# Kernel optimization log

Measured on AMD Instinct MI355X. Metric: run time of the kernel, lower is better.

The kernel has to match this reference:

```python
import jax, jax.numpy as jnp
import numpy as np

DIM = 768
NUM_HEADS = 12
HEAD_DIM = DIM // NUM_HEADS  # 64


def setup_inputs() -> dict:
    key = jax.random.key(0)
    k1, k2, k3, k4 = jax.random.split(key, 4)
    B, N = 2, 2048
    x = jax.random.normal(k1, (B, N, DIM), dtype=jnp.float32)
    att_mask = jnp.ones((B, N), dtype=jnp.int32)
    # learned params (qkv has no bias since qkv_bias=False)
    qkv_w = jax.random.normal(k2, (3 * DIM, DIM), dtype=jnp.float32) * (1.0 / np.sqrt(DIM))
    proj_w = jax.random.normal(k3, (DIM, DIM), dtype=jnp.float32) * (1.0 / np.sqrt(DIM))
    proj_b = jax.random.normal(k4, (DIM,), dtype=jnp.float32) * 0.02
    return {"x": x, "att_mask": att_mask, "qkv_w": qkv_w, "proj_w": proj_w, "proj_b": proj_b}


def reference(x, att_mask, qkv_w, proj_w, proj_b):
    B, N, C = x.shape
    H, Dh = NUM_HEADS, HEAD_DIM
    scale = Dh ** (-0.5)
    # qkv projection: [B,N,3C] -> [3,B,H,N,Dh]
    qkv = jnp.einsum('bnc,oc->bno', x, qkv_w)
    qkv = qkv.reshape(B, N, 3, H, Dh).transpose(2, 0, 3, 1, 4)
    q, k, v = qkv[0], qkv[1], qkv[2]
    q = q * scale
    # full N x N logits (the memory-bound hotspot)
    logit = jnp.einsum('bhnd,bhmd->bhnm', q, k)
    # 2D mask path: [B,N] -> [B,1,1,N], masked_fill(mask==0, -inf)
    mask = att_mask[:, None, None, :]
    logit = jnp.where(mask == 0, -jnp.inf, logit)
    attn = jax.nn.softmax(logit, axis=-1)  # attn_drop is identity (p=0, eval)
    out = jnp.einsum('bhnm,bhmd->bhnd', attn, v)
    out = out.transpose(0, 2, 1, 3).reshape(B, N, H * Dh)
    out = jnp.einsum('bnc,oc->bno', out, proj_w) + proj_b  # proj_drop identity
    return out
```

## Files before the change

kernel.cpp:

```cpp
#include <hip/hip_runtime.h>
#include <hip/hip_bf16.h>
#include <math.h>
#include <cstdint>
#include <cstddef>

typedef __bf16 bf16x8 __attribute__((ext_vector_type(8)));
typedef __bf16 bf16x4 __attribute__((ext_vector_type(4)));
typedef short  s16x4  __attribute__((ext_vector_type(4)));
typedef float  f32x4  __attribute__((ext_vector_type(4)));

#define GLOAD16(g, l) __builtin_amdgcn_global_load_lds( \
    (const __attribute__((address_space(1))) void*)(g),  \
    (__attribute__((address_space(3))) void*)(l), 16, 0, 0)

__device__ __forceinline__ unsigned short f2bf(float f) {
    union { float f; unsigned u; } v; v.f = f;
    unsigned u = v.u;
    u += 0x7fffu + ((u >> 16) & 1u);
    return (unsigned short)(u >> 16);
}

__device__ __forceinline__ unsigned pack_bf16x2(float a, float b) {
    __hip_bfloat162 h = __float22bfloat162_rn(make_float2(a, b));
    return *reinterpret_cast<unsigned*>(&h);
}

__device__ __forceinline__ f32x4 mfma16(bf16x4 a, bf16x4 b, f32x4 c) {
#if __has_builtin(__builtin_amdgcn_mfma_f32_16x16x16_bf16)
    return __builtin_amdgcn_mfma_f32_16x16x16_bf16(a, b, c, 0, 0, 0);
#elif __has_builtin(__builtin_amdgcn_mfma_f32_16x16x16bf16_1k)
    return __builtin_amdgcn_mfma_f32_16x16x16bf16_1k(
        __builtin_bit_cast(s16x4, a), __builtin_bit_cast(s16x4, b), c, 0, 0, 0);
#else
    asm volatile("v_mfma_f32_16x16x16_bf16 %0, %1, %2, %0"
                 : "+v"(c) : "v"(a), "v"(b));
    return c;
#endif
}

__global__ __launch_bounds__(256) void cvt_all(
    const float* __restrict__ x,
    const float* __restrict__ qkvw,
    const float* __restrict__ projw,
    unsigned short* __restrict__ xb,
    unsigned short* __restrict__ wqkv,
    unsigned short* __restrict__ wproj)
{
    const int N1 = 4096 * 768;
    const int N2 = 2304 * 768;
    const int SC = 768 * 768;
    const float C2 = 0.18033688011112042f;
    int i = ((int)blockIdx.x * 256 + (int)threadIdx.x) * 4;

    const float* src;
    unsigned short* dst;
    int j;
    bool sc = false;
    if (i < N1)           { src = x;     dst = xb;    j = i; }
    else if (i < N1 + N2) { j = i - N1;  src = qkvw;  dst = wqkv;  sc = (j < SC); }
    else                  { j = i - N1 - N2; src = projw; dst = wproj; }

    float4 v = *reinterpret_cast<const float4*>(src + j);
    if (sc) { v.x *= C2; v.y *= C2; v.z *= C2; v.w *= C2; }
    uint2 pk;
    pk.x = pack_bf16x2(v.x, v.y);
    pk.y = pack_bf16x2(v.z, v.w);
    *reinterpret_cast<uint2*>(dst + j) = pk;
}

template <int MODE, int MROWS, int NF>
__global__ __launch_bounds__(256) void gemm_bt(
    const unsigned short* __restrict__ A,
    const unsigned short* __restrict__ B,
    unsigned short* __restrict__ Cb,
    unsigned short* __restrict__ Vt,
    float* __restrict__ Cf,
    const float* __restrict__ bias,
    int M, int N, int K)
{
    constexpr int MI = MROWS / 32;
    __shared__ __align__(16) unsigned short Al[2][MROWS * 64];
    __shared__ __align__(16) unsigned short Bl[2][NF * 32 * 64];
    const int bm   = blockIdx.x * MROWS;
    const int bn   = blockIdx.y * (NF * 32);
    const int tid  = (int)threadIdx.x;
    const int wave = tid >> 6;
    const int lane = tid & 63;
    const int wr   = wave >> 1;
    const int wc   = wave & 1;
    const int q    = lane & 15;
    const int g4   = (lane >> 4) * 4;

    f32x4 acc[MI][NF] = {};

    const int srow = lane >> 3;
    const int scol = (lane & 7) * 8;

    auto stage = [&](int buf, int k0) {
#pragma unroll
        for (int i = 0; i < MI; ++i) {
            const int chunk = wave * MI + i;
            GLOAD16(A + (size_t)(bm + chunk * 8 + srow) * K + (k0 + scol),
                    &Al[buf][chunk * 512]);
        }
#pragma unroll
        for (int i = 0; i < NF; ++i) {
            const int chunk = wave * NF + i;
            GLOAD16(B + (size_t)(bn + chunk * 8 + srow) * K + (k0 + scol),
                    &Bl[buf][chunk * 512]);
        }
    };

    stage(0, 0);
    __syncthreads();

    const int nt = K / 64;
    int buf = 0;
    for (int t = 0; t < nt; ++t) {
        if (t + 1 < nt) stage(buf ^ 1, (t + 1) * 64);
#pragma unroll
        for (int kk = 0; kk < 2; ++kk) {
            const int ko = kk * 32 + (lane >> 4) * 8;
            bf16x8 af[MI], bf[NF];
#pragma unroll
            for (int mi = 0; mi < MI; ++mi)
                af[mi] = *(const bf16x8*)&Al[buf][(wr * (MROWS / 2) + mi * 16 + q) * 64 + ko];
#pragma unroll
            for (int ni = 0; ni < NF; ++ni)
                bf[ni] = *(const bf16x8*)&Bl[buf][(wc * 16 * NF + ni * 16 + q) * 64 + ko];
#pragma unroll
            for (int mi = 0; mi < MI; ++mi)
#pragma unroll
                for (int ni = 0; ni < NF; ++ni)
                    acc[mi][ni] = __builtin_amdgcn_mfma_f32_16x16x32_bf16(
                        af[mi], bf[ni], acc[mi][ni], 0, 0, 0);
        }
        __syncthreads();
        buf ^= 1;
    }

#pragma unroll
    for (int mi = 0; mi < MI; ++mi) {
        const int row0 = bm + wr * (MROWS / 2) + mi * 16 + g4;
        if constexpr (MODE == 1) {
#pragma unroll
            for (int ni = 0; ni < NF; ++ni) {
                const int col = bn + wc * 16 * NF + ni * 16 + q;
#pragma unroll
                for (int r = 0; r < 4; ++r)
                    Cf[(size_t)(row0 + r) * N + col] = acc[mi][ni][r] + bias[col];
            }
        } else {
            if (bn < 1536) {
#pragma unroll
                for (int ni = 0; ni < NF; ++ni) {
                    const int col = bn + wc * 16 * NF + ni * 16 + q;
#pragma unroll
                    for (int r = 0; r < 4; ++r)
                        Cb[(size_t)(row0 + r) * 1536 + col] = f2bf(acc[mi][ni][r]);
                }
            } else {
                const int b  = row0 >> 11;
                const int np = row0 & 2047;
#pragma unroll
                for (int ni = 0; ni < NF; ++ni) {
                    const int vcol = bn + wc * 16 * NF + ni * 16 + q - 1536;
                    const int hv = vcol >> 6, d = vcol & 63;
                    uint2 w;
                    w.x = pack_bf16x2(acc[mi][ni][0], acc[mi][ni][1]);
                    w.y = pack_bf16x2(acc[mi][ni][2], acc[mi][ni][3]);
                    *reinterpret_cast<uint2*>(
                        &Vt[((size_t)(b * 12 + hv) * 64 + d) * 2048 + np]) = w;
                }
            }
        }
    }
}

__global__ __launch_bounds__(256, 3) void attn_fwd(
    const unsigned short* __restrict__ qk,
    const unsigned short* __restrict__ vT,
    const int* __restrict__ mask,
    unsigned short* __restrict__ out)
{
    const int NN = 2048, H = 12;
    const int bh = (int)blockIdx.y;
    const int b  = bh / H, h = bh % H;
    const int q0 = (int)blockIdx.x * 64;
    const int tid = (int)threadIdx.x, wave = tid >> 6, lane = tid & 63;
    const int g   = lane >> 4;
    const int q   = lane & 15;
    const int swz = (q & 7) << 3;

    __shared__ __align__(16) unsigned short LDS[16896];
    unsigned short* Kl0 = LDS;
    unsigned short* Vl0 = LDS + 8192;

    bool allone;
    {
        const int* mrow = mask + b * NN + lane * 32;
        unsigned mv = 0xFFFFFFFFu;
#pragma unroll
        for (int i = 0; i < 8; ++i) {
            int4 m = *reinterpret_cast<const int4*>(mrow + i * 4);
            mv = min(mv, min(min((unsigned)m.x, (unsigned)m.y),
                             min((unsigned)m.z, (unsigned)m.w)));
        }
        allone = __all(mv != 0u);
    }

    bf16x8 qf[2][4];
#pragma unroll
    for (int kk = 0; kk < 2; ++kk)
#pragma unroll
        for (int qt = 0; qt < 4; ++qt)
            qf[kk][qt] = *reinterpret_cast<const bf16x8*>(
                &qk[(size_t)(b * NN + q0 + 16 * qt + q) * 1536 + h * 64 + kk * 32 + g * 8]);

    const char* kg0 = (const char*)(qk + (size_t)(b * NN + wave * 16 + (lane >> 3)) * 1536
                                    + 768 + h * 64 + ((lane & 7) ^ (lane >> 3)) * 8);
    const char* kg1 = kg0 + (size_t)8 * 1536 * 2;
    const unsigned short* vgp = vT + (size_t)(bh * 64 + (lane >> 1)) * 2048
                                + 16 * wave + (lane & 1) * 8;

    auto stageK = [&](int buf) {
        GLOAD16(kg0, &Kl0[buf * 4096 + wave * 1024]);
        GLOAD16(kg1, &Kl0[buf * 4096 + wave * 1024 + 512]);
        kg0 += (size_t)64 * 1536 * 2;
        kg1 += (size_t)64 * 1536 * 2;
    };
    auto stageV = [&](int buf) {
        GLOAD16(vgp,                     &Vl0[buf * 4096 + wave * 1024]);
        GLOAD16(vgp + (size_t)32 * 2048, &Vl0[buf * 4096 + wave * 1024 + 512]);
        vgp += 64;
    };

    f32x4 oacc[4][4] = {};
    float l[4] = {0.f, 0.f, 0.f, 0.f};

    stageV(0); stageK(0);

    int cur = 0;
    for (int it = 0; it < 32; ++it) {
        if (it < 31) { stageV(cur ^ 1); stageK(cur ^ 1); }

        if (it < 31) asm volatile("s_waitcnt vmcnt(4)" ::: "memory");
        else         asm volatile("s_waitcnt vmcnt(0)" ::: "memory");

        f32x4 s[4] = {};
        __builtin_amdgcn_s_setprio(1);
#pragma unroll
        for (int kk = 0; kk < 2; ++kk) {
            bf16x8 kf = *(const bf16x8*)&Kl0[cur * 4096 + (16 * wave + q) * 64
                                             + ((kk * 32 + g * 8) ^ swz)];
#pragma unroll
            for (int qt = 0; qt < 4; ++qt)
                s[qt] = __builtin_amdgcn_mfma_f32_16x16x32_bf16(kf, qf[kk][qt], s[qt], 0, 0, 0);
        }
        __builtin_amdgcn_s_setprio(0);

        if (!allone) {
            int4 mr = *reinterpret_cast<const int4*>(
                &mask[b * NN + it * 64 + 16 * wave + 4 * g]);
#pragma unroll
            for (int qt = 0; qt < 4; ++qt) {
                if (mr.x == 0) s[qt][0] = -INFINITY;
                if (mr.y == 0) s[qt][1] = -INFINITY;
                if (mr.z == 0) s[qt][2] = -INFINITY;
                if (mr.w == 0) s[qt][3] = -INFINITY;
            }
        }

        bf16x4 pb[4];
#pragma unroll
        for (int qt = 0; qt < 4; ++qt) {
            float p0 = __builtin_amdgcn_exp2f(s[qt][0]);
            float p1 = __builtin_amdgcn_exp2f(s[qt][1]);
            float p2 = __builtin_amdgcn_exp2f(s[qt][2]);
            float p3 = __builtin_amdgcn_exp2f(s[qt][3]);
            l[qt] += (p0 + p1) + (p2 + p3);
            uint2 t;
            t.x = pack_bf16x2(p0, p1);
            t.y = pack_bf16x2(p2, p3);
            pb[qt] = __builtin_bit_cast(bf16x4, t);
        }

        __builtin_amdgcn_s_setprio(1);
#pragma unroll
        for (int ct = 0; ct < 4; ++ct) {
            bf16x4 va = *(const bf16x4*)&Vl0[cur * 4096 + wave * 1024
                                             + (16 * ct + q) * 16 + 4 * g];
#pragma unroll
            for (int qt = 0; qt < 4; ++qt)
                oacc[ct][qt] = mfma16(va, pb[qt], oacc[ct][qt]);
        }
        __builtin_amdgcn_s_setprio(0);

        cur ^= 1;
    }

    __syncthreads();

#pragma unroll
    for (int qt = 0; qt < 4; ++qt) {
        l[qt] += __shfl_xor(l[qt], 16);
        l[qt] += __shfl_xor(l[qt], 32);
    }
    float* lb = (float*)&LDS[16384];
    float* fb = (float*)&LDS[0];
    if (g == 0) {
#pragma unroll
        for (int qt = 0; qt < 4; ++qt) lb[wave * 64 + qt * 16 + q] = l[qt];
    }
    if (wave & 1) {
        float* dst = fb + (wave >> 1) * 4096;
#pragma unroll
        for (int ct = 0; ct < 4; ++ct)
#pragma unroll
            for (int qt = 0; qt < 4; ++qt)
                *reinterpret_cast<f32x4*>(&dst[(ct * 4 + qt) * 256 + lane * 4]) = oacc[ct][qt];
    }
    __syncthreads();
    if (!(wave & 1)) {
        float* srcp = fb + (wave >> 1) * 4096;
#pragma unroll
        for (int ct = 0; ct < 4; ++ct)
#pragma unroll
            for (int qt = 0; qt < 4; ++qt)
                oacc[ct][qt] += *reinterpret_cast<f32x4*>(&srcp[(ct * 4 + qt) * 256 + lane * 4]);
    }
    __syncthreads();
    if (wave == 2) {
#pragma unroll
        for (int ct = 0; ct < 4; ++ct)
#pragma unroll
            for (int qt = 0; qt < 4; ++qt)
                *reinterpret_cast<f32x4*>(&fb[(ct * 4 + qt) * 256 + lane * 4]) = oacc[ct][qt];
    }
    __syncthreads();
    if (wave == 0) {
        float inv[4];
#pragma unroll
        for (int qt = 0; qt < 4; ++qt)
            inv[qt] = 1.0f / (lb[qt * 16 + q] + lb[64 + qt * 16 + q]
                              + lb[128 + qt * 16 + q] + lb[192 + qt * 16 + q]);
#pragma unroll
        for (int ct = 0; ct < 4; ++ct)
#pragma unroll
            for (int qt = 0; qt < 4; ++qt) {
                f32x4 o = oacc[ct][qt]
                        + *reinterpret_cast<f32x4*>(&fb[(ct * 4 + qt) * 256 + lane * 4]);
                uint2 ow;
                ow.x = pack_bf16x2(o[0] * inv[qt], o[1] * inv[qt]);
                ow.y = pack_bf16x2(o[2] * inv[qt], o[3] * inv[qt]);
                *reinterpret_cast<uint2*>(
                    &out[(size_t)(b * NN + q0 + 16 * qt + q) * 768 + h * 64 + 16 * ct + 4 * g]) = ow;
            }
    }
}

extern "C" void kernel_launch(void* const* d_in, const int* in_sizes, int n_in,
                              void* d_out, int out_size, void* d_ws, size_t ws_size,
                              hipStream_t stream)
{
    const float* x      = (const float*)d_in[0];
    const int*   mask   = (const int*)d_in[1];
    const float* qkv_w  = (const float*)d_in[2];
    const float* proj_w = (const float*)d_in[3];
    const float* proj_b = (const float*)d_in[4];
    float* out = (float*)d_out;

    const int BN = 2 * 2048;
    const int C  = 768;
    const int C3 = 2304;

    char* w = (char*)d_ws;
    unsigned short* xb    = (unsigned short*)w; w += (size_t)BN * C    * 2;
    unsigned short* wqkv  = (unsigned short*)w; w += (size_t)C3 * C    * 2;
    unsigned short* wproj = (unsigned short*)w; w += (size_t)C  * C    * 2;
    unsigned short* qk    = (unsigned short*)w; w += (size_t)BN * 1536 * 2;
    unsigned short* vT    = (unsigned short*)w; w += (size_t)24 * 64 * 2048 * 2;
    unsigned short* ao    = (unsigned short*)w;

    {
        const int total = (BN * C + C3 * C + C * C) / 4;
        cvt_all<<<total / 256, 256, 0, stream>>>(x, qkv_w, proj_w, xb, wqkv, wproj);
    }

    gemm_bt<2, 128, 4><<<dim3(BN / 128, C3 / 128), 256, 0, stream>>>(
        xb, wqkv, qk, vT, nullptr, nullptr, BN, C3, C);

    attn_fwd<<<dim3(2048 / 64, 24), 256, 0, stream>>>(qk, vT, mask, ao);

    gemm_bt<1, 128, 2><<<dim3(BN / 128, C / 64), 256, 0, stream>>>(
        ao, wproj, nullptr, nullptr, out, proj_b, BN, C, C);
}
```

Before: 110.0 us.

## Pre-tile V layout, remap attention grid for XCD locality, split waitcnt

The QKV GEMM epilogue now writes V in a pre-tiled layout matching the attention kernel's per-wave LDS tile, so each wave stages V with contiguous 1 KB loads instead of strided rows. The attention grid becomes 1D with a block-to-head mapping that groups each head's query tiles onto the same XCD (bid&7), aiming to improve K/V L2 reuse. K is now issued before V and the wait is split, so QK^T and softmax start before V arrives. The output projection GEMM also uses a smaller M tile to launch more blocks.

```diff
diff --git a/kernel.cpp b/kernel.cpp
--- a/kernel.cpp
+++ b/kernel.cpp
@@ -160,17 +160,22 @@
                         Cb[(size_t)(row0 + r) * 1536 + col] = f2bf(acc[mi][ni][r]);
                 }
             } else {
-                const int b  = row0 >> 11;
-                const int np = row0 & 2047;
+                const int bb  = row0 >> 11;
+                const int np  = row0 & 2047;
+                const int tt  = np >> 6;
+                const int wv  = (np >> 4) & 3;
+                const int gg  = (np >> 2) & 3;
 #pragma unroll
                 for (int ni = 0; ni < NF; ++ni) {
                     const int vcol = bn + wc * 16 * NF + ni * 16 + q - 1536;
                     const int hv = vcol >> 6, d = vcol & 63;
+                    const size_t idx =
+                        ((size_t)((bb * 12 + hv) * 32 + tt) * 4 + wv) * 1024
+                        + gg * 256 + d * 4;
                     uint2 w;
                     w.x = pack_bf16x2(acc[mi][ni][0], acc[mi][ni][1]);
                     w.y = pack_bf16x2(acc[mi][ni][2], acc[mi][ni][3]);
-                    *reinterpret_cast<uint2*>(
-                        &Vt[((size_t)(b * 12 + hv) * 64 + d) * 2048 + np]) = w;
+                    *reinterpret_cast<uint2*>(&Vt[idx]) = w;
                 }
             }
         }
@@ -184,9 +189,11 @@
     unsigned short* __restrict__ out)
 {
     const int NN = 2048, H = 12;
-    const int bh = (int)blockIdx.y;
-    const int b  = bh / H, h = bh % H;
-    const int q0 = (int)blockIdx.x * 64;
+    const int bid = (int)blockIdx.x;
+    const int bhh = (bid & 7) * 3 + ((bid >> 3) >> 5);
+    const int qt  = (bid >> 3) & 31;
+    const int b   = bhh / H, h = bhh % H;
+    const int q0  = qt * 64;
     const int tid = (int)threadIdx.x, wave = tid >> 6, lane = tid & 63;
     const int g   = lane >> 4;
     const int q   = lane & 15;
@@ -213,15 +220,14 @@
 #pragma unroll
     for (int kk = 0; kk < 2; ++kk)
 #pragma unroll
-        for (int qt = 0; qt < 4; ++qt)
-            qf[kk][qt] = *reinterpret_cast<const bf16x8*>(
-                &qk[(size_t)(b * NN + q0 + 16 * qt + q) * 1536 + h * 64 + kk * 32 + g * 8]);
+        for (int qtl = 0; qtl < 4; ++qtl)
+            qf[kk][qtl] = *reinterpret_cast<const bf16x8*>(
+                &qk[(size_t)(b * NN + q0 + 16 * qtl + q) * 1536 + h * 64 + kk * 32 + g * 8]);
 
     const char* kg0 = (const char*)(qk + (size_t)(b * NN + wave * 16 + (lane >> 3)) * 1536
                                     + 768 + h * 64 + ((lane & 7) ^ (lane >> 3)) * 8);
     const char* kg1 = kg0 + (size_t)8 * 1536 * 2;
-    const unsigned short* vgp = vT + (size_t)(bh * 64 + (lane >> 1)) * 2048
-                                + 16 * wave + (lane & 1) * 8;
+    const unsigned short* vgp = vT + ((size_t)bhh * 32 * 4 + wave) * 1024 + lane * 8;
 
     auto stageK = [&](int buf) {
         GLOAD16(kg0, &Kl0[buf * 4096 + wave * 1024]);
@@ -230,22 +236,22 @@
         kg1 += (size_t)64 * 1536 * 2;
     };
     auto stageV = [&](int buf) {
-        GLOAD16(vgp,                     &Vl0[buf * 4096 + wave * 1024]);
-        GLOAD16(vgp + (size_t)32 * 2048, &Vl0[buf * 4096 + wave * 1024 + 512]);
-        vgp += 64;
+        GLOAD16(vgp,       &Vl0[buf * 4096 + wave * 1024]);
+        GLOAD16(vgp + 512, &Vl0[buf * 4096 + wave * 1024 + 512]);
+        vgp += 4096;
     };
 
     f32x4 oacc[4][4] = {};
     float l[4] = {0.f, 0.f, 0.f, 0.f};
 
-    stageV(0); stageK(0);
+    stageK(0); stageV(0);
 
     int cur = 0;
     for (int it = 0; it < 32; ++it) {
-        if (it < 31) { stageV(cur ^ 1); stageK(cur ^ 1); }
-
-        if (it < 31) asm volatile("s_waitcnt vmcnt(4)" ::: "memory");
-        else         asm volatile("s_waitcnt vmcnt(0)" ::: "memory");
+        if (it < 31) { stageK(cur ^ 1); stageV(cur ^ 1); }
+
+        if (it < 31) asm volatile("s_waitcnt vmcnt(6)" ::: "memory");
+        else         asm volatile("s_waitcnt vmcnt(2)" ::: "memory");
 
         f32x4 s[4] = {};
         __builtin_amdgcn_s_setprio(1);
@@ -254,8 +260,8 @@
             bf16x8 kf = *(const bf16x8*)&Kl0[cur * 4096 + (16 * wave + q) * 64
                                              + ((kk * 32 + g * 8) ^ swz)];
 #pragma unroll
-            for (int qt = 0; qt < 4; ++qt)
-                s[qt] = __builtin_amdgcn_mfma_f32_16x16x32_bf16(kf, qf[kk][qt], s[qt], 0, 0, 0);
+            for (int qtl = 0; qtl < 4; ++qtl)
+                s[qtl] = __builtin_amdgcn_mfma_f32_16x16x32_bf16(kf, qf[kk][qtl], s[qtl], 0, 0, 0);
         }
         __builtin_amdgcn_s_setprio(0);
 
@@ -263,36 +269,39 @@
             int4 mr = *reinterpret_cast<const int4*>(
                 &mask[b * NN + it * 64 + 16 * wave + 4 * g]);
 #pragma unroll
-            for (int qt = 0; qt < 4; ++qt) {
-                if (mr.x == 0) s[qt][0] = -INFINITY;
-                if (mr.y == 0) s[qt][1] = -INFINITY;
-                if (mr.z == 0) s[qt][2] = -INFINITY;
-                if (mr.w == 0) s[qt][3] = -INFINITY;
+            for (int qtl = 0; qtl < 4; ++qtl) {
+                if (mr.x == 0) s[qtl][0] = -INFINITY;
+                if (mr.y == 0) s[qtl][1] = -INFINITY;
+                if (mr.z == 0) s[qtl][2] = -INFINITY;
+                if (mr.w == 0) s[qtl][3] = -INFINITY;
             }
         }
 
         bf16x4 pb[4];
 #pragma unroll
-        for (int qt = 0; qt < 4; ++qt) {
-            float p0 = __builtin_amdgcn_exp2f(s[qt][0]);
-            float p1 = __builtin_amdgcn_exp2f(s[qt][1]);
-            float p2 = __builtin_amdgcn_exp2f(s[qt][2]);
-            float p3 = __builtin_amdgcn_exp2f(s[qt][3]);
-            l[qt] += (p0 + p1) + (p2 + p3);
+        for (int qtl = 0; qtl < 4; ++qtl) {
+            float p0 = __builtin_amdgcn_exp2f(s[qtl][0]);
+            float p1 = __builtin_amdgcn_exp2f(s[qtl][1]);
+            float p2 = __builtin_amdgcn_exp2f(s[qtl][2]);
+            float p3 = __builtin_amdgcn_exp2f(s[qtl][3]);
+            l[qtl] += (p0 + p1) + (p2 + p3);
             uint2 t;
             t.x = pack_bf16x2(p0, p1);
             t.y = pack_bf16x2(p2, p3);
-            pb[qt] = __builtin_bit_cast(bf16x4, t);
-        }
+            pb[qtl] = __builtin_bit_cast(bf16x4, t);
+        }
+
+        if (it < 31) asm volatile("s_waitcnt vmcnt(4)" ::: "memory");
+        else         asm volatile("s_waitcnt vmcnt(0)" ::: "memory");
 
         __builtin_amdgcn_s_setprio(1);
 #pragma unroll
         for (int ct = 0; ct < 4; ++ct) {
             bf16x4 va = *(const bf16x4*)&Vl0[cur * 4096 + wave * 1024
-                                             + (16 * ct + q) * 16 + 4 * g];
-#pragma unroll
-            for (int qt = 0; qt < 4; ++qt)
-                oacc[ct][qt] = mfma16(va, pb[qt], oacc[ct][qt]);
+                                             + g * 256 + (16 * ct + q) * 4];
+#pragma unroll
+            for (int qtl = 0; qtl < 4; ++qtl)
+                oacc[ct][qtl] = mfma16(va, pb[qtl], oacc[ct][qtl]);
         }
         __builtin_amdgcn_s_setprio(0);
 
@@ -302,23 +311,23 @@
     __syncthreads();
 
 #pragma unroll
-    for (int qt = 0; qt < 4; ++qt) {
-        l[qt] += __shfl_xor(l[qt], 16);
-        l[qt] += __shfl_xor(l[qt], 32);
+    for (int qtl = 0; qtl < 4; ++qtl) {
+        l[qtl] += __shfl_xor(l[qtl], 16);
+        l[qtl] += __shfl_xor(l[qtl], 32);
     }
     float* lb = (float*)&LDS[16384];
     float* fb = (float*)&LDS[0];
     if (g == 0) {
 #pragma unroll
-        for (int qt = 0; qt < 4; ++qt) lb[wave * 64 + qt * 16 + q] = l[qt];
+        for (int qtl = 0; qtl < 4; ++qtl) lb[wave * 64 + qtl * 16 + q] = l[qtl];
     }
     if (wave & 1) {
         float* dst = fb + (wave >> 1) * 4096;
 #pragma unroll
         for (int ct = 0; ct < 4; ++ct)
 #pragma unroll
-            for (int qt = 0; qt < 4; ++qt)
-                *reinterpret_cast<f32x4*>(&dst[(ct * 4 + qt) * 256 + lane * 4]) = oacc[ct][qt];
+            for (int qtl = 0; qtl < 4; ++qtl)
+                *reinterpret_cast<f32x4*>(&dst[(ct * 4 + qtl) * 256 + lane * 4]) = oacc[ct][qtl];
     }
     __syncthreads();
     if (!(wave & 1)) {
@@ -326,35 +335,35 @@
 #pragma unroll
         for (int ct = 0; ct < 4; ++ct)
 #pragma unroll
-            for (int qt = 0; qt < 4; ++qt)
-                oacc[ct][qt] += *reinterpret_cast<f32x4*>(&srcp[(ct * 4 + qt) * 256 + lane * 4]);
+            for (int qtl = 0; qtl < 4; ++qtl)
+                oacc[ct][qtl] += *reinterpret_cast<f32x4*>(&srcp[(ct * 4 + qtl) * 256 + lane * 4]);
     }
     __syncthreads();
     if (wave == 2) {
 #pragma unroll
         for (int ct = 0; ct < 4; ++ct)
 #pragma unroll
-            for (int qt = 0; qt < 4; ++qt)
-                *reinterpret_cast<f32x4*>(&fb[(ct * 4 + qt) * 256 + lane * 4]) = oacc[ct][qt];
+            for (int qtl = 0; qtl < 4; ++qtl)
+                *reinterpret_cast<f32x4*>(&fb[(ct * 4 + qtl) * 256 + lane * 4]) = oacc[ct][qtl];
     }
     __syncthreads();
     if (wave == 0) {
         float inv[4];
 #pragma unroll
-        for (int qt = 0; qt < 4; ++qt)
-            inv[qt] = 1.0f / (lb[qt * 16 + q] + lb[64 + qt * 16 + q]
-                              + lb[128 + qt * 16 + q] + lb[192 + qt * 16 + q]);
+        for (int qtl = 0; qtl < 4; ++qtl)
+            inv[qtl] = 1.0f / (lb[qtl * 16 + q] + lb[64 + qtl * 16 + q]
+                              + lb[128 + qtl * 16 + q] + lb[192 + qtl * 16 + q]);
 #pragma unroll
         for (int ct = 0; ct < 4; ++ct)
 #pragma unroll
-            for (int qt = 0; qt < 4; ++qt) {
-                f32x4 o = oacc[ct][qt]
-                        + *reinterpret_cast<f32x4*>(&fb[(ct * 4 + qt) * 256 + lane * 4]);
+            for (int qtl = 0; qtl < 4; ++qtl) {
+                f32x4 o = oacc[ct][qtl]
+                        + *reinterpret_cast<f32x4*>(&fb[(ct * 4 + qtl) * 256 + lane * 4]);
                 uint2 ow;
-                ow.x = pack_bf16x2(o[0] * inv[qt], o[1] * inv[qt]);
-                ow.y = pack_bf16x2(o[2] * inv[qt], o[3] * inv[qt]);
+                ow.x = pack_bf16x2(o[0] * inv[qtl], o[1] * inv[qtl]);
+                ow.y = pack_bf16x2(o[2] * inv[qtl], o[3] * inv[qtl]);
                 *reinterpret_cast<uint2*>(
-                    &out[(size_t)(b * NN + q0 + 16 * qt + q) * 768 + h * 64 + 16 * ct + 4 * g]) = ow;
+                    &out[(size_t)(b * NN + q0 + 16 * qtl + q) * 768 + h * 64 + 16 * ct + 4 * g]) = ow;
             }
     }
 }
@@ -390,8 +399,8 @@
     gemm_bt<2, 128, 4><<<dim3(BN / 128, C3 / 128), 256, 0, stream>>>(
         xb, wqkv, qk, vT, nullptr, nullptr, BN, C3, C);
 
-    attn_fwd<<<dim3(2048 / 64, 24), 256, 0, stream>>>(qk, vT, mask, ao);
-
-    gemm_bt<1, 128, 2><<<dim3(BN / 128, C / 64), 256, 0, stream>>>(
+    attn_fwd<<<dim3(768), 256, 0, stream>>>(qk, vT, mask, ao);
+
+    gemm_bt<1, 64, 2><<<dim3(BN / 64, C / 64), 256, 0, stream>>>(
         ao, wproj, nullptr, nullptr, out, proj_b, BN, C, C);
 }
```

Result: faster. 105.1 us (-4.5%).
